# Kernel optimization log

Hardware: AMD Instinct MI355X
Metric: run time of the kernel (lower is better)

The kernel has to match this reference:

```python
import jax, jax.numpy as jnp
import numpy as np

EMBED_DIM = 1024
NUM_HEADS = 16
HEAD_DIM = EMBED_DIM // NUM_HEADS
ALPHA = 0.5  # mirror_bias['alpha'] default


def setup_inputs() -> dict:
    key = jax.random.key(0)
    k_x, k_m, kq, kk, kv, ko = jax.random.split(key, 6)
    B, S = 2, 2048
    x = jax.random.normal(k_x, (B, S, EMBED_DIM), dtype=jnp.float32)
    mask = jax.random.bernoulli(k_m, 0.1, (B, S))  # True = masked-out key (padding)
    # xavier_uniform for square [E,E]: limit = sqrt(6/(E+E))
    lim = float(np.sqrt(6.0 / (EMBED_DIM + EMBED_DIM)))
    Wq = jax.random.uniform(kq, (EMBED_DIM, EMBED_DIM), jnp.float32, -lim, lim)
    Wk = jax.random.uniform(kk, (EMBED_DIM, EMBED_DIM), jnp.float32, -lim, lim)
    Wv = jax.random.uniform(kv, (EMBED_DIM, EMBED_DIM), jnp.float32, -lim, lim)
    Wo = jax.random.uniform(ko, (EMBED_DIM, EMBED_DIM), jnp.float32, -lim, lim)
    return {"x": x, "Wq": Wq, "Wk": Wk, "Wv": Wv, "Wo": Wo, "mask": mask}


def _heads(t, B, S):
    # [B,S,E] -> [B,H,S,D]
    return t.reshape(B, S, NUM_HEADS, HEAD_DIM).transpose(0, 2, 1, 3)


def reference(x, Wq, Wk, Wv, Wo, mask):
    B, S, E = x.shape
    # nn.Linear(bias=False): y = x @ W.T
    q = _heads(x @ Wq.T, B, S)
    k = _heads(x @ Wk.T, B, S)
    v = _heads(x @ Wv.T, B, S)
    scores = jnp.einsum('bhqd,bhkd->bhqk', q, k) / jnp.sqrt(jnp.float32(HEAD_DIM))
    # mirror positional bias: target j = S-1-i
    i_idx = jnp.arange(S)[:, None]
    j_idx = jnp.arange(S)[None, :]
    dist = jnp.abs(j_idx - (S - 1 - i_idx)).astype(jnp.float32)
    bias = -ALPHA * (dist / jnp.float32(S))  # [S_q, S_k]
    scores = scores + bias[None, None, :, :]
    # bool 2D mask -> key padding mask [B,1,1,S_k], True = -inf
    scores = jnp.where(mask[:, None, None, :], -jnp.inf, scores)
    attn = jax.nn.softmax(scores, axis=-1)
    out = jnp.einsum('bhqk,bhkd->bhqd', attn, v)
    out = out.transpose(0, 2, 1, 3).reshape(B, S, E)
    return out @ Wo.T
```

## Files before the change

### kernel.cpp

```cpp
#include <hip/hip_runtime.h>

typedef unsigned short u16;
typedef unsigned int u32;
typedef unsigned long long u64;
typedef __attribute__((ext_vector_type(8))) short bf16x8;
typedef __attribute__((ext_vector_type(4))) float f32x4;
typedef __attribute__((ext_vector_type(2))) unsigned int u32x2;

#define MFMA16(A, B, C) __builtin_amdgcn_mfma_f32_16x16x32_bf16(A, B, C, 0, 0, 0)

__device__ __forceinline__ u16 f2bf(float f) {
  union { float f; unsigned u; } x; x.f = f;
  unsigned r = x.u + 0x7fffu + ((x.u >> 16) & 1u);
  return (u16)(r >> 16);
}

__device__ __forceinline__ u32 pack_bf2(float a, float b) {
  const u32 ua = __builtin_bit_cast(u32, a) + 0x8000u;
  const u32 ub = __builtin_bit_cast(u32, b) + 0x8000u;
  return __builtin_amdgcn_perm(ub, ua, 0x07060302u);
}

__device__ __forceinline__ void gload_lds16(const u16* g, u16* l) {
  __builtin_amdgcn_global_load_lds((const __attribute__((address_space(1))) void*)g,
                                   (__attribute__((address_space(3))) void*)l,
                                   16, 0, 0);
}

__global__ __launch_bounds__(256) void cvt_all(const float* __restrict__ x,
                                               const float* __restrict__ Wq,
                                               const float* __restrict__ Wk,
                                               const float* __restrict__ Wv,
                                               const float* __restrict__ Wo,
                                               const int* __restrict__ mask,
                                               u16* __restrict__ xb,
                                               u16* __restrict__ Wqkvb,
                                               u16* __restrict__ Wob,
                                               u32* __restrict__ mbits,
                                               int NE, int NW, int NB) {
  if ((int)blockIdx.x == NB) {
    const int t = threadIdx.x;
    if (t < 128) {
      const int* m = mask + t * 32;
      u32 w = 0;
#pragma unroll
      for (int j = 0; j < 32; j++) w |= (m[j] != 0 ? 1u : 0u) << j;
      mbits[t] = w;
    }
    return;
  }
  const int e = (blockIdx.x * 256 + threadIdx.x) * 8;
  const float* s;
  u16* d;
  if (e < NE) { s = x + e; d = xb + e; }
  else {
    int f = e - NE;
    if (f < 3 * NW) {
      d = Wqkvb + f;
      s = (f < NW) ? Wq + f : (f < 2 * NW) ? Wk + (f - NW) : Wv + (f - 2 * NW);
    } else { f -= 3 * NW; s = Wo + f; d = Wob + f; }
  }
  const float4 a = *(const float4*)s;
  const float4 b = *(const float4*)(s + 4);
  bf16x8 o;
  o[0] = (short)f2bf(a.x); o[1] = (short)f2bf(a.y);
  o[2] = (short)f2bf(a.z); o[3] = (short)f2bf(a.w);
  o[4] = (short)f2bf(b.x); o[5] = (short)f2bf(b.y);
  o[6] = (short)f2bf(b.z); o[7] = (short)f2bf(b.w);
  *(bf16x8*)d = o;
}

__global__ __launch_bounds__(256) void gemm_qkv(const u16* __restrict__ A,
                                                const u16* __restrict__ B,
                                                u16* __restrict__ Qo,
                                                u16* __restrict__ Ko,
                                                u16* __restrict__ Vto,
                                                int M, int N, int K) {
  __shared__ alignas(16) u16 As[128 * 32];
  __shared__ alignas(16) u16 Bs[128 * 32];
  const int t = threadIdx.x;
  const int lane = t & 63, wave = t >> 6;
  const int quad = lane >> 4, l16 = lane & 15;
  const int m0 = blockIdx.y * 128, n0 = blockIdx.x * 128;
  const int wm = (wave >> 1) * 64, wn = (wave & 1) * 64;

  f32x4 acc[4][4] = {};

  for (int kk = 0; kk < K; kk += 32) {
#pragma unroll
    for (int i = 0; i < 2; i++) {
      const int l = t + i * 256;
      const int row = l >> 2, c8 = (l & 3) * 8;
      gload_lds16(A + (size_t)(m0 + row) * K + kk + c8, As + (size_t)l * 8);
      gload_lds16(B + (size_t)(n0 + row) * K + kk + c8, Bs + (size_t)l * 8);
    }
    __syncthreads();

    bf16x8 af[4], bfr[4];
#pragma unroll
    for (int i = 0; i < 4; i++)
      af[i] = *(const bf16x8*)(As + (wm + i * 16 + l16) * 32 + quad * 8);
#pragma unroll
    for (int j = 0; j < 4; j++)
      bfr[j] = *(const bf16x8*)(Bs + (wn + j * 16 + l16) * 32 + quad * 8);
#pragma unroll
    for (int i = 0; i < 4; i++)
#pragma unroll
      for (int j = 0; j < 4; j++)
        acc[i][j] = MFMA16(af[i], bfr[j], acc[i][j]);
    __syncthreads();
  }

  const int G = ((m0 + wm) & 2047) >> 6;
#pragma unroll
  for (int j = 0; j < 4; j++) {
    const int col = n0 + wn + j * 16 + l16;
    if (col < 1024) {
#pragma unroll
      for (int i = 0; i < 4; i++)
#pragma unroll
        for (int r = 0; r < 4; r++)
          Qo[(size_t)(m0 + wm + i * 16 + quad * 4 + r) * 1024 + col] =
              f2bf(acc[i][j][r]);
    } else if (col < 2048) {
#pragma unroll
      for (int i = 0; i < 4; i++)
#pragma unroll
        for (int r = 0; r < 4; r++)
          Ko[(size_t)(m0 + wm + i * 16 + quad * 4 + r) * 1024 + (col - 1024)] =
              f2bf(acc[i][j][r]);
    } else {
      u16* base = Vto + ((size_t)(m0 >> 11) * 1024 + (col - 2048)) * 2048 + G * 64;
#pragma unroll
      for (int r = 0; r < 4; r++) {
        u32x2 v;
        v.x = pack_bf2(acc[0][j][r], acc[1][j][r]);
        v.y = pack_bf2(acc[2][j][r], acc[3][j][r]);
        *(u32x2*)(base + 4 * (quad * 4 + r)) = v;
      }
    }
  }
}

__global__ __launch_bounds__(256) void gemm_out(const u16* __restrict__ A,
                                                const u16* __restrict__ B,
                                                float* __restrict__ C,
                                                int M, int N, int K) {
  __shared__ alignas(16) u16 As[128 * 32];
  __shared__ alignas(16) u16 Bs[64 * 32];
  const int t = threadIdx.x;
  const int lane = t & 63, wave = t >> 6;
  const int quad = lane >> 4, l16 = lane & 15;
  const int m0 = blockIdx.y * 128, n0 = blockIdx.x * 64;
  const int wm = (wave >> 1) * 64, wn = (wave & 1) * 32;

  f32x4 acc[4][2] = {};

  for (int kk = 0; kk < K; kk += 32) {
#pragma unroll
    for (int i = 0; i < 2; i++) {
      const int l = t + i * 256;
      const int row = l >> 2, c8 = (l & 3) * 8;
      gload_lds16(A + (size_t)(m0 + row) * K + kk + c8, As + (size_t)l * 8);
    }
    {
      gload_lds16(B + (size_t)(n0 + (t >> 2)) * K + kk + (t & 3) * 8,
                  Bs + (size_t)t * 8);
    }
    __syncthreads();

    bf16x8 af[4], bfr[2];
#pragma unroll
    for (int i = 0; i < 4; i++)
      af[i] = *(const bf16x8*)(As + (wm + i * 16 + l16) * 32 + quad * 8);
#pragma unroll
    for (int j = 0; j < 2; j++)
      bfr[j] = *(const bf16x8*)(Bs + (wn + j * 16 + l16) * 32 + quad * 8);
#pragma unroll
    for (int i = 0; i < 4; i++)
#pragma unroll
      for (int j = 0; j < 2; j++)
        acc[i][j] = MFMA16(af[i], bfr[j], acc[i][j]);
    __syncthreads();
  }

#pragma unroll
  for (int i = 0; i < 4; i++)
#pragma unroll
    for (int j = 0; j < 2; j++)
#pragma unroll
      for (int r = 0; r < 4; r++)
        C[(size_t)(m0 + wm + i * 16 + quad * 4 + r) * N + n0 + wn + j * 16 + l16] =
            acc[i][j][r];
}

__global__ __launch_bounds__(256) void attn_fwd(const u16* __restrict__ Q,
                                                const u16* __restrict__ Kb_,
                                                const u16* __restrict__ Vt,
                                                const u32* __restrict__ mbits,
                                                float* __restrict__ OP0,
                                                float* __restrict__ OP1,
                                                float* __restrict__ Lp) {
  constexpr int S = 2048, E = 1024;
  __shared__ alignas(16) u16 Ks[2][64 * 64];
  __shared__ alignas(16) u16 Vs[2][64 * 64];
  __shared__ alignas(16) u32 Pl[4][16 * 32];
  const int t = threadIdx.x;
  const int lane = t & 63, wave = t >> 6;
  const int quad = lane >> 4, l16 = lane & 15;
  const int bh = blockIdx.y, b = bh >> 4, h = bh & 15;
  const int sp = blockIdx.z;
  const int kbase0 = sp * 1024;
  const int q0 = blockIdx.x * 128 + wave * 32;

  const int c0 = t, c1 = t + 256;
  const int kr0 = c0 >> 3, kr1 = c1 >> 3;
  const int kcol0 = ((c0 & 7) ^ (kr0 & 7)) * 8;
  const int kcol1 = ((c1 & 7) ^ (kr1 & 7)) * 8;
  const u16* kP0 = Kb_ + (size_t)(b * S + kbase0 + kr0) * E + h * 64 + kcol0;
  const u16* kP1 = Kb_ + (size_t)(b * S + kbase0 + kr1) * E + h * 64 + kcol1;
  const u16* vbase = Vt + (size_t)(b * 16 + h) * 64 * S + kbase0;
  const u16* vP0 = vbase + (size_t)kr0 * S + kcol0;
  const u16* vP1 = vbase + (size_t)kr1 * S + kcol1;

  bf16x8 aq[2][2];
#pragma unroll
  for (int qt = 0; qt < 2; qt++) {
    const u16* qp = Q + ((size_t)(b * S) + q0 + qt * 16 + l16) * E + h * 64;
    aq[qt][0] = *(const bf16x8*)(qp + quad * 8);
    aq[qt][1] = *(const bf16x8*)(qp + 32 + quad * 8);
  }

  const u32* mb = mbits + b * 64;
  const int sx = l16 & 7;
  const int pkey = l16 & 14;

  float lr[2][4] = {};
  f32x4 accO[2][4] = {};
  const float fq0 = (float)(q0 + quad * 4 - 2047);

  const float K1 = 0.125f * 1.44269504f;
  const float K2 = 2.44140625e-4f * 1.44269504f;
  const float K3 = -8.0f * 1.44269504f;

  gload_lds16(kP0, Ks[0] + c0 * 8);
  gload_lds16(kP1, Ks[0] + c1 * 8);
  gload_lds16(vP0, Vs[0] + c0 * 8);
  gload_lds16(vP1, Vs[0] + c1 * 8);
  __syncthreads();

  int buf = 0;
  for (int kc = 0; kc < 1024; kc += 64) {
    if (kc + 64 < 1024) {
      const int kn = kc + 64;
      gload_lds16(kP0 + (size_t)kn * E, Ks[buf ^ 1] + c0 * 8);
      gload_lds16(kP1 + (size_t)kn * E, Ks[buf ^ 1] + c1 * 8);
      gload_lds16(vP0 + kn, Vs[buf ^ 1] + c0 * 8);
      gload_lds16(vP1 + kn, Vs[buf ^ 1] + c1 * 8);
    }
    const u16* ks = Ks[buf];
    const u16* vs = Vs[buf];
    u32* pl = Pl[wave];

    bf16x8 bk[4][2];
#pragma unroll
    for (int T = 0; T < 4; T++)
#pragma unroll
      for (int dh = 0; dh < 2; dh++)
        bk[T][dh] = *(const bf16x8*)(ks + (T * 16 + l16) * 64 +
                                     ((dh * 4 + quad) ^ sx) * 8);

    f32x4 s[2][4] = {};
#pragma unroll
    for (int qt = 0; qt < 2; qt++)
#pragma unroll
      for (int T = 0; T < 4; T++) {
        s[qt][T] = MFMA16(aq[qt][0], bk[T][0], s[qt][T]);
        s[qt][T] = MFMA16(aq[qt][1], bk[T][1], s[qt][T]);
      }

    const int kabs = kbase0 + kc;
    const u64 mw = *(const u64*)(mb + (kabs >> 5));
    const u32 mlo = (u32)mw, mhi = (u32)(mw >> 32);
    const int mk0 = (mlo >> l16) & 1, mk1 = (mlo >> (l16 + 16)) & 1;
    const int mk2 = (mhi >> l16) & 1, mk3 = (mhi >> (l16 + 16)) & 1;
    const float kl = (float)(kabs + l16);

    u32x2 pk1[4];
#pragma unroll
    for (int qt = 0; qt < 2; qt++)
#pragma unroll
      for (int r = 0; r < 4; r++) {
        const float fb = kl + fq0 + (float)(qt * 16 + r);
        const float e0 = fmaf(fabsf(fb), -K2, fmaf(s[qt][0][r], K1, K3));
        const float e1 = fmaf(fabsf(fb + 16.f), -K2, fmaf(s[qt][1][r], K1, K3));
        const float e2 = fmaf(fabsf(fb + 32.f), -K2, fmaf(s[qt][2][r], K1, K3));
        const float e3 = fmaf(fabsf(fb + 48.f), -K2, fmaf(s[qt][3][r], K1, K3));
        const float p0 = mk0 ? 0.f : __builtin_amdgcn_exp2f(e0);
        const float p1 = mk1 ? 0.f : __builtin_amdgcn_exp2f(e1);
        const float p2 = mk2 ? 0.f : __builtin_amdgcn_exp2f(e2);
        const float p3 = mk3 ? 0.f : __builtin_amdgcn_exp2f(e3);
        lr[qt][r] += (p0 + p1) + (p2 + p3);
        u32x2 v;
        v.x = pack_bf2(p0, p1);
        v.y = pack_bf2(p2, p3);
        if (qt == 0) {
          const int m = quad * 4 + r;
          *(u32x2*)(pl + m * 32 + 2 * (l16 ^ (m & 14))) = v;
        } else {
          pk1[r] = v;
        }
      }

    bf16x8 bv[2][4];
#pragma unroll
    for (int kst = 0; kst < 2; kst++)
#pragma unroll
      for (int tt = 0; tt < 4; tt++)
        bv[kst][tt] = *(const bf16x8*)(vs + (tt * 16 + l16) * 64 +
                                       ((kst * 4 + quad) ^ sx) * 8);

    asm volatile("s_waitcnt lgkmcnt(0)" ::: "memory");
    bf16x8 ap0[2];
#pragma unroll
    for (int kst = 0; kst < 2; kst++)
      ap0[kst] = *(const bf16x8*)(pl + l16 * 32 + 2 * ((kst * 8 + 2 * quad) ^ pkey));
#pragma unroll
    for (int kst = 0; kst < 2; kst++)
#pragma unroll
      for (int tt = 0; tt < 4; tt++)
        accO[0][tt] = MFMA16(ap0[kst], bv[kst][tt], accO[0][tt]);

    asm volatile("" ::: "memory");
#pragma unroll
    for (int r = 0; r < 4; r++) {
      const int m = quad * 4 + r;
      *(u32x2*)(pl + m * 32 + 2 * (l16 ^ (m & 14))) = pk1[r];
    }
    asm volatile("s_waitcnt lgkmcnt(0)" ::: "memory");
    bf16x8 ap1[2];
#pragma unroll
    for (int kst = 0; kst < 2; kst++)
      ap1[kst] = *(const bf16x8*)(pl + l16 * 32 + 2 * ((kst * 8 + 2 * quad) ^ pkey));
#pragma unroll
    for (int kst = 0; kst < 2; kst++)
#pragma unroll
      for (int tt = 0; tt < 4; tt++)
        accO[1][tt] = MFMA16(ap1[kst], bv[kst][tt], accO[1][tt]);

    __syncthreads();
    buf ^= 1;
  }

  float* OP = sp ? OP1 : OP0;
#pragma unroll
  for (int qt = 0; qt < 2; qt++)
#pragma unroll
    for (int r = 0; r < 4; r++) {
      float l = lr[qt][r];
      l += __shfl_xor(l, 1);
      l += __shfl_xor(l, 2);
      l += __shfl_xor(l, 4);
      l += __shfl_xor(l, 8);
      const int qg = q0 + qt * 16 + quad * 4 + r;
      const size_t row = ((size_t)bh << 11) + qg;
      float* orow = OP + row * 64;
#pragma unroll
      for (int tt = 0; tt < 4; tt++) orow[tt * 16 + l16] = accO[qt][tt][r];
      if (l16 == 0) Lp[((size_t)sp << 16) + row] = l;
    }
}

__global__ __launch_bounds__(256) void attn_merge(const float* __restrict__ OP0,
                                                  const float* __restrict__ OP1,
                                                  const float* __restrict__ Lp,
                                                  u16* __restrict__ Ao) {
  const int i = blockIdx.x * 256 + threadIdx.x;
  const int row = i >> 4;
  const int d4 = (i & 15) * 4;
  const float inv = 1.0f / (Lp[row] + Lp[65536 + row]);
  const float4 a = *(const float4*)(OP0 + (size_t)row * 64 + d4);
  const float4 c = *(const float4*)(OP1 + (size_t)row * 64 + d4);
  const int bb = row >> 15, h = (row >> 11) & 15, q = row & 2047;
  u32x2 v;
  v.x = pack_bf2((a.x + c.x) * inv, (a.y + c.y) * inv);
  v.y = pack_bf2((a.z + c.z) * inv, (a.w + c.w) * inv);
  *(u32x2*)(Ao + (size_t)((bb << 11) + q) * 1024 + h * 64 + d4) = v;
}

extern "C" void kernel_launch(void* const* d_in, const int* in_sizes, int n_in,
                              void* d_out, int out_size, void* d_ws, size_t ws_size,
                              hipStream_t stream) {
  const float* x  = (const float*)d_in[0];
  const float* Wq = (const float*)d_in[1];
  const float* Wk = (const float*)d_in[2];
  const float* Wv = (const float*)d_in[3];
  const float* Wo = (const float*)d_in[4];
  const int* mask = (const int*)d_in[5];

  const int M = 4096, N = 1024, K = 1024;
  const int NE = M * N, NW = N * K;
  const int NB = (NE + 4 * NW) / 2048;

  u16* xb    = (u16*)d_ws;
  u16* Wqkvb = xb + NE;
  u16* Wob   = Wqkvb + (size_t)3 * NW;
  u16* Qb    = Wob + NW;
  u16* Kb    = Qb + NE;
  u16* Vt    = Kb + NE;
  u16* Ao    = Vt + NE;
  u32* mbits = (u32*)(Ao + NE);
  float* OP1 = (float*)(mbits + 128);
  float* Lp  = OP1 + (size_t)65536 * 64;
  float* OP0 = (float*)d_out;

  cvt_all<<<NB + 1, 256, 0, stream>>>(x, Wq, Wk, Wv, Wo, mask,
                                      xb, Wqkvb, Wob, mbits, NE, NW, NB);

  gemm_qkv<<<dim3(3072 / 128, M / 128), 256, 0, stream>>>(
      xb, Wqkvb, Qb, Kb, Vt, M, 3072, K);
  attn_fwd<<<dim3(16, 32, 2), 256, 0, stream>>>(Qb, Kb, Vt, mbits,
                                                OP0, OP1, Lp);
  attn_merge<<<4096, 256, 0, stream>>>(OP0, OP1, Lp, Ao);
  gemm_out<<<dim3(N / 64, M / 128), 256, 0, stream>>>(
      Ao, Wob, (float*)d_out, M, N, K);
}
```

Before: 217.6 us.

## Fuse split-KV attention merge into output GEMM and use swizzled K=64 tiles

Removes the separate attn_merge kernel. The output projection GEMM now reads the two fp32 partial attention outputs and their row sums directly, normalizes them, converts to bf16 and writes its A tile into LDS, so the intermediate bf16 Ao buffer is no longer needed. Both GEMMs move from a K step of 32 to 64 with an XOR-swizzled LDS layout, which halves the number of barriers and is meant to avoid bank conflicts. In exchange, the output GEMM re-reads fp32 partials (twice the bytes of bf16) for every column block, and the non-async A-tile loads are no longer overlapped.

```diff
diff --git a/kernel.cpp b/kernel.cpp
--- a/kernel.cpp
+++ b/kernel.cpp
@@ -6,6 +6,7 @@
 typedef __attribute__((ext_vector_type(8))) short bf16x8;
 typedef __attribute__((ext_vector_type(4))) float f32x4;
 typedef __attribute__((ext_vector_type(2))) unsigned int u32x2;
+typedef __attribute__((ext_vector_type(4))) unsigned int u32x4;
 
 #define MFMA16(A, B, C) __builtin_amdgcn_mfma_f32_16x16x32_bf16(A, B, C, 0, 0, 0)
 
@@ -76,38 +77,45 @@
                                                 u16* __restrict__ Ko,
                                                 u16* __restrict__ Vto,
                                                 int M, int N, int K) {
-  __shared__ alignas(16) u16 As[128 * 32];
-  __shared__ alignas(16) u16 Bs[128 * 32];
+  __shared__ alignas(16) u16 As[128 * 64];
+  __shared__ alignas(16) u16 Bs[128 * 64];
   const int t = threadIdx.x;
   const int lane = t & 63, wave = t >> 6;
   const int quad = lane >> 4, l16 = lane & 15;
   const int m0 = blockIdx.y * 128, n0 = blockIdx.x * 128;
   const int wm = (wave >> 1) * 64, wn = (wave & 1) * 64;
+  const int sx = l16 & 7;
 
   f32x4 acc[4][4] = {};
 
-  for (int kk = 0; kk < K; kk += 32) {
-#pragma unroll
-    for (int i = 0; i < 2; i++) {
-      const int l = t + i * 256;
-      const int row = l >> 2, c8 = (l & 3) * 8;
-      gload_lds16(A + (size_t)(m0 + row) * K + kk + c8, As + (size_t)l * 8);
-      gload_lds16(B + (size_t)(n0 + row) * K + kk + c8, Bs + (size_t)l * 8);
+  for (int kk = 0; kk < K; kk += 64) {
+#pragma unroll
+    for (int i = 0; i < 4; i++) {
+      const int c = t + i * 256;
+      const int row = c >> 3, sub = c & 7;
+      const int col = ((sub ^ (row & 7)) * 8);
+      gload_lds16(A + (size_t)(m0 + row) * K + kk + col, As + (size_t)c * 8);
+      gload_lds16(B + (size_t)(n0 + row) * K + kk + col, Bs + (size_t)c * 8);
     }
     __syncthreads();
 
-    bf16x8 af[4], bfr[4];
-#pragma unroll
-    for (int i = 0; i < 4; i++)
-      af[i] = *(const bf16x8*)(As + (wm + i * 16 + l16) * 32 + quad * 8);
-#pragma unroll
-    for (int j = 0; j < 4; j++)
-      bfr[j] = *(const bf16x8*)(Bs + (wn + j * 16 + l16) * 32 + quad * 8);
-#pragma unroll
-    for (int i = 0; i < 4; i++)
+#pragma unroll
+    for (int ks = 0; ks < 2; ks++) {
+      bf16x8 af[4], bfr[4];
+#pragma unroll
+      for (int i = 0; i < 4; i++)
+        af[i] = *(const bf16x8*)(As + (wm + i * 16 + l16) * 64 +
+                                 ((ks * 4 + quad) ^ sx) * 8);
 #pragma unroll
       for (int j = 0; j < 4; j++)
-        acc[i][j] = MFMA16(af[i], bfr[j], acc[i][j]);
+        bfr[j] = *(const bf16x8*)(Bs + (wn + j * 16 + l16) * 64 +
+                                  ((ks * 4 + quad) ^ sx) * 8);
+#pragma unroll
+      for (int i = 0; i < 4; i++)
+#pragma unroll
+        for (int j = 0; j < 4; j++)
+          acc[i][j] = MFMA16(af[i], bfr[j], acc[i][j]);
+    }
     __syncthreads();
   }
 
@@ -142,45 +150,73 @@
   }
 }
 
-__global__ __launch_bounds__(256) void gemm_out(const u16* __restrict__ A,
-                                                const u16* __restrict__ B,
+__global__ __launch_bounds__(256) void gemm_out(const float* __restrict__ OP0,
+                                                const float* __restrict__ OP1,
+                                                const float* __restrict__ Lp,
+                                                const u16* __restrict__ Bw,
                                                 float* __restrict__ C,
                                                 int M, int N, int K) {
-  __shared__ alignas(16) u16 As[128 * 32];
-  __shared__ alignas(16) u16 Bs[64 * 32];
+  __shared__ alignas(16) u16 As[128 * 64];
+  __shared__ alignas(16) u16 Bs[64 * 64];
   const int t = threadIdx.x;
   const int lane = t & 63, wave = t >> 6;
   const int quad = lane >> 4, l16 = lane & 15;
   const int m0 = blockIdx.y * 128, n0 = blockIdx.x * 64;
   const int wm = (wave >> 1) * 64, wn = (wave & 1) * 32;
+  const int sx = l16 & 7;
+
+  const int arow = t >> 1, ah = t & 1;
+  const int bq16 = ((m0 + arow) >> 11) * 16;
+  const int qq = (m0 + arow) & 2047;
 
   f32x4 acc[4][2] = {};
 
-  for (int kk = 0; kk < K; kk += 32) {
+  for (int kk = 0; kk < 1024; kk += 64) {
+    const int h = kk >> 6;
+    const size_t r64 = (((size_t)(bq16 + h)) << 11) + qq;
+    const float inv = 1.0f / (Lp[r64] + Lp[65536 + r64]);
+    const float* p0 = OP0 + r64 * 64 + ah * 32;
+    const float* p1 = OP1 + r64 * 64 + ah * 32;
+#pragma unroll
+    for (int j = 0; j < 4; j++) {
+      const float4 a  = *(const float4*)(p0 + j * 8);
+      const float4 a2 = *(const float4*)(p0 + j * 8 + 4);
+      const float4 c  = *(const float4*)(p1 + j * 8);
+      const float4 c2 = *(const float4*)(p1 + j * 8 + 4);
+      u32x4 w;
+      w.x = pack_bf2((a.x + c.x) * inv, (a.y + c.y) * inv);
+      w.y = pack_bf2((a.z + c.z) * inv, (a.w + c.w) * inv);
+      w.z = pack_bf2((a2.x + c2.x) * inv, (a2.y + c2.y) * inv);
+      w.w = pack_bf2((a2.z + c2.z) * inv, (a2.w + c2.w) * inv);
+      const int sub = ah * 4 + j;
+      *(u32x4*)(As + ((size_t)arow * 8 + (sub ^ (arow & 7))) * 8) = w;
+    }
 #pragma unroll
     for (int i = 0; i < 2; i++) {
-      const int l = t + i * 256;
-      const int row = l >> 2, c8 = (l & 3) * 8;
-      gload_lds16(A + (size_t)(m0 + row) * K + kk + c8, As + (size_t)l * 8);
-    }
-    {
-      gload_lds16(B + (size_t)(n0 + (t >> 2)) * K + kk + (t & 3) * 8,
-                  Bs + (size_t)t * 8);
+      const int c = t + i * 256;
+      const int row = c >> 3, sub = c & 7;
+      gload_lds16(Bw + (size_t)(n0 + row) * K + kk + ((sub ^ (row & 7)) * 8),
+                  Bs + (size_t)c * 8);
     }
     __syncthreads();
 
-    bf16x8 af[4], bfr[2];
-#pragma unroll
-    for (int i = 0; i < 4; i++)
-      af[i] = *(const bf16x8*)(As + (wm + i * 16 + l16) * 32 + quad * 8);
-#pragma unroll
-    for (int j = 0; j < 2; j++)
-      bfr[j] = *(const bf16x8*)(Bs + (wn + j * 16 + l16) * 32 + quad * 8);
-#pragma unroll
-    for (int i = 0; i < 4; i++)
+#pragma unroll
+    for (int ks = 0; ks < 2; ks++) {
+      bf16x8 af[4], bfr[2];
+#pragma unroll
+      for (int i = 0; i < 4; i++)
+        af[i] = *(const bf16x8*)(As + (wm + i * 16 + l16) * 64 +
+                                 ((ks * 4 + quad) ^ sx) * 8);
 #pragma unroll
       for (int j = 0; j < 2; j++)
-        acc[i][j] = MFMA16(af[i], bfr[j], acc[i][j]);
+        bfr[j] = *(const bf16x8*)(Bs + (wn + j * 16 + l16) * 64 +
+                                  ((ks * 4 + quad) ^ sx) * 8);
+#pragma unroll
+      for (int i = 0; i < 4; i++)
+#pragma unroll
+        for (int j = 0; j < 2; j++)
+          acc[i][j] = MFMA16(af[i], bfr[j], acc[i][j]);
+    }
     __syncthreads();
   }
 
@@ -371,23 +407,6 @@
     }
 }
 
-__global__ __launch_bounds__(256) void attn_merge(const float* __restrict__ OP0,
-                                                  const float* __restrict__ OP1,
-                                                  const float* __restrict__ Lp,
-                                                  u16* __restrict__ Ao) {
-  const int i = blockIdx.x * 256 + threadIdx.x;
-  const int row = i >> 4;
-  const int d4 = (i & 15) * 4;
-  const float inv = 1.0f / (Lp[row] + Lp[65536 + row]);
-  const float4 a = *(const float4*)(OP0 + (size_t)row * 64 + d4);
-  const float4 c = *(const float4*)(OP1 + (size_t)row * 64 + d4);
-  const int bb = row >> 15, h = (row >> 11) & 15, q = row & 2047;
-  u32x2 v;
-  v.x = pack_bf2((a.x + c.x) * inv, (a.y + c.y) * inv);
-  v.y = pack_bf2((a.z + c.z) * inv, (a.w + c.w) * inv);
-  *(u32x2*)(Ao + (size_t)((bb << 11) + q) * 1024 + h * 64 + d4) = v;
-}
-
 extern "C" void kernel_launch(void* const* d_in, const int* in_sizes, int n_in,
                               void* d_out, int out_size, void* d_ws, size_t ws_size,
                               hipStream_t stream) {
@@ -408,11 +427,10 @@
   u16* Qb    = Wob + NW;
   u16* Kb    = Qb + NE;
   u16* Vt    = Kb + NE;
-  u16* Ao    = Vt + NE;
-  u32* mbits = (u32*)(Ao + NE);
-  float* OP1 = (float*)(mbits + 128);
+  u32* mbits = (u32*)(Vt + NE);
+  float* OP0 = (float*)(mbits + 128);
+  float* OP1 = OP0 + (size_t)65536 * 64;
   float* Lp  = OP1 + (size_t)65536 * 64;
-  float* OP0 = (float*)d_out;
 
   cvt_all<<<NB + 1, 256, 0, stream>>>(x, Wq, Wk, Wv, Wo, mask,
                                       xb, Wqkvb, Wob, mbits, NE, NW, NB);
@@ -421,7 +439,6 @@
       xb, Wqkvb, Qb, Kb, Vt, M, 3072, K);
   attn_fwd<<<dim3(16, 32, 2), 256, 0, stream>>>(Qb, Kb, Vt, mbits,
                                                 OP0, OP1, Lp);
-  attn_merge<<<4096, 256, 0, stream>>>(OP0, OP1, Lp, Ao);
   gemm_out<<<dim3(N / 64, M / 128), 256, 0, stream>>>(
-      Ao, Wob, (float*)d_out, M, N, K);
-}
+      OP0, OP1, Lp, Wob, (float*)d_out, M, N, K);
+}
```

After: 265.2 us. 1.22x slower.
